# Kernel optimization log

Measured on AMD Instinct MI355X. Metric: run time of the kernel, lower is better.

Reference implementation:

```python
import jax, jax.numpy as jnp
import numpy as np

N = 50000
E = 800000
D_IN = 96
D_OUT = 128


def setup_inputs() -> dict:
    key = jax.random.key(0)
    k1, k2, k3, k4, k5 = jax.random.split(key, 5)
    x = jax.random.normal(k1, (N, D_IN), dtype=jnp.float32)
    edge_index = jax.random.randint(k2, (2, E), 0, N, dtype=jnp.int32)
    s = 1.0 / np.sqrt(D_IN)
    # lin_l: applied to aggregated neighbor features (has bias in PyG SAGEConv)
    W_l = jax.random.uniform(k3, (D_OUT, D_IN), jnp.float32, -s, s)
    b_l = jax.random.uniform(k4, (D_OUT,), jnp.float32, -s, s)
    # lin_r: root/self weight (no bias)
    W_r = jax.random.uniform(k5, (D_OUT, D_IN), jnp.float32, -s, s)
    return {"x": x, "edge_index": edge_index, "W_l": W_l, "b_l": b_l, "W_r": W_r}


def reference(x, edge_index, W_l, b_l, W_r):
    src, dst = edge_index[0], edge_index[1]
    # gather source features, mean-aggregate onto targets
    msg = x[src]  # [E, D_IN]
    summed = jax.ops.segment_sum(msg, dst, num_segments=N)  # [N, D_IN]
    count = jax.ops.segment_sum(jnp.ones((E,), x.dtype), dst, num_segments=N)
    agg = summed / jnp.maximum(count, 1.0)[:, None]
    # SAGEConv: lin_l(agg) + lin_r(x), then layer-level ReLU
    out = agg @ W_l.T + b_l + x @ W_r.T
    return jax.nn.relu(out)
```

## Files before the change

### kernel.cpp

```cpp
#include <hip/hip_runtime.h>
#include <hip/hip_bf16.h>

#define N_NODES 50000
#define N_EDGES 800000
#define D_IN 96
#define D_OUT 128
#define CAP 64

#define N_BINS 256
#define NODES_PER_BIN 196
#define BIN_CAP 4096
#define TAIL_STRIDE 16

#define PART_EPB 3125
#define PART_BLOCKS (N_EDGES / PART_EPB)
#define PART_SLOTS 13

#define CONV_THREADS (N_NODES * 12)
#define CONV_BLOCKS ((CONV_THREADS + 255) / 256)
#define WCONV_BLOCKS 12

#define SLICES 8
#define NODES_PER_SLICE 6250
#define NPB 64
#define SLICE_AG_BLOCKS ((NODES_PER_SLICE + NPB - 1) / NPB)
#define AG_BLOCKS (SLICES * SLICE_AG_BLOCKS)
#define AH_PITCH 104

typedef unsigned short u16;
typedef __attribute__((ext_vector_type(8))) short short8;
typedef __attribute__((ext_vector_type(4))) float f32x4;

__device__ __forceinline__ u16 f2bf(float f) {
    unsigned u = __float_as_uint(f);
    unsigned r = (u + 0x7FFFu + ((u >> 16) & 1u)) >> 16;
    return (u16)r;
}
__device__ __forceinline__ float bf2f(u16 h) {
    return __uint_as_float(((unsigned)h) << 16);
}

__global__ __launch_bounds__(256) void sage_part_conv(
    const int* __restrict__ src,
    const int* __restrict__ dst,
    const float* __restrict__ x,
    const float* __restrict__ Wl,
    const float* __restrict__ Wr,
    int* __restrict__ tail,
    unsigned* __restrict__ binbuf,
    u16* __restrict__ xh,
    u16* __restrict__ Wfrag)
{
    __shared__ unsigned hist[N_BINS];
    __shared__ unsigned base[N_BINS];
    __shared__ unsigned cur[N_BINS];

    const int b = blockIdx.x;
    const int tid = (int)threadIdx.x;

    if (b < PART_BLOCKS) {
        hist[tid] = 0u; cur[tid] = 0u;
        __syncthreads();

        const int ebase = b * PART_EPB;
        const int e0 = ebase + tid;
        int d[PART_SLOTS], s[PART_SLOTS], bn[PART_SLOTS];
#pragma unroll
        for (int i = 0; i < PART_SLOTS; i++) {
            int valid = (tid + i * 256) < PART_EPB;
            int e = valid ? (e0 + i * 256) : ebase;
            d[i] = dst[e];
            s[i] = src[e];
        }
#pragma unroll
        for (int i = 0; i < PART_SLOTS; i++) {
            bn[i] = d[i] / NODES_PER_BIN;
            if ((tid + i * 256) < PART_EPB)
                atomicAdd(&hist[bn[i]], 1u);
        }
        __syncthreads();
        base[tid] = (unsigned)atomicAdd(&tail[tid * TAIL_STRIDE], (int)hist[tid]);
        __syncthreads();
#pragma unroll
        for (int i = 0; i < PART_SLOTS; i++) {
            if ((tid + i * 256) < PART_EPB) {
                unsigned loc = atomicAdd(&cur[bn[i]], 1u);
                unsigned pos = base[bn[i]] + loc;
                unsigned dl = (unsigned)(d[i] - bn[i] * NODES_PER_BIN);
                if (pos < BIN_CAP)
                    binbuf[(unsigned)bn[i] * BIN_CAP + pos] =
                        (dl << 16) | (unsigned)s[i];
            }
        }
    } else if (b < PART_BLOCKS + CONV_BLOCKS) {
        unsigned t = (unsigned)(b - PART_BLOCKS) * 256u + threadIdx.x;
        if (t >= (unsigned)CONV_THREADS) return;
        unsigned n = t / 12u;
        unsigned c8 = t - n * 12u;
        const float* p = x + (size_t)n * D_IN + c8 * 8u;
        short8 v;
#pragma unroll
        for (int i = 0; i < 8; i++) v[i] = (short)f2bf(p[i]);
        *(short8*)(xh + (size_t)n * D_IN + c8 * 8u) = v;
    } else {
        int idx = (b - PART_BLOCKS - CONV_BLOCKS) * 256 + tid;
        int j = idx / 24;
        int c8 = idx - j * 24;
        int kc = c8 >> 2;
        int quad = c8 & 3;
        const float* wsrc = (c8 < 12) ? (Wl + (size_t)j * D_IN + c8 * 8)
                                      : (Wr + (size_t)j * D_IN + (c8 - 12) * 8);
        int jt = j >> 4;
        int col = j & 15;
        short8 v;
#pragma unroll
        for (int i = 0; i < 8; i++) v[i] = (short)f2bf(wsrc[i]);
        *(short8*)(Wfrag + (((jt * 6 + kc) * 64) + col + 16 * quad) * 8) = v;
    }
}

__global__ __launch_bounds__(256) void sage_bin(
    const int* __restrict__ tail,
    const unsigned* __restrict__ binbuf,
    int* __restrict__ cursor,
    u16* __restrict__ bucket)
{
    __shared__ __align__(16) u16 bkt[NODES_PER_BIN * CAP];
    __shared__ unsigned cnt[NODES_PER_BIN];

    const int j = blockIdx.x;
    const int tid = (int)threadIdx.x;
    const int nbase = j * NODES_PER_BIN;
    const int nvalid = (N_NODES - nbase) < NODES_PER_BIN ? (N_NODES - nbase)
                                                         : NODES_PER_BIN;

    for (int r = tid; r < NODES_PER_BIN; r += 256) cnt[r] = 0u;
    __syncthreads();

    int TAIL = tail[j * TAIL_STRIDE];
    if (TAIL > BIN_CAP) TAIL = BIN_CAP;
    const unsigned* sb = binbuf + (size_t)j * BIN_CAP;

    for (int e0 = tid * 4; e0 < TAIL; e0 += 1024) {
        uint4 v = *(const uint4*)(sb + e0);
        unsigned vv0 = v.x, vv1 = v.y, vv2 = v.z, vv3 = v.w;
#pragma unroll
        for (int k = 0; k < 4; k++) {
            unsigned w = (k == 0) ? vv0 : (k == 1) ? vv1 : (k == 2) ? vv2 : vv3;
            if (e0 + k < TAIL) {
                unsigned r = w >> 16;
                if (r < NODES_PER_BIN) {
                    unsigned p = atomicAdd(&cnt[r], 1u);
                    if (p < CAP) bkt[r * CAP + p] = (u16)(w & 0xFFFFu);
                }
            }
        }
    }
    __syncthreads();

    for (int idx = tid; idx < nvalid * 8; idx += 256) {
        int r = idx >> 3, q = idx & 7;
        *(short8*)(bucket + (size_t)(nbase + r) * CAP + q * 8) =
            *(const short8*)(bkt + r * CAP + q * 8);
    }
    for (int r = tid; r < nvalid; r += 256)
        cursor[nbase + r] = (int)cnt[r];
}

__global__ __launch_bounds__(256) void sage_agg_gemm(
    const u16* __restrict__ xh,
    const int* __restrict__ cursor,
    const u16* __restrict__ bucket,
    const u16* __restrict__ Wfrag,
    const float* __restrict__ bl,
    float* __restrict__ out)
{
    __shared__ u16 Ah[NPB * AH_PITCH];

    const int tid = threadIdx.x;
    const int g = blockIdx.x & 7;
    const int kblk = blockIdx.x >> 3;
    const int n0 = g * NODES_PER_SLICE + kblk * NPB;
    const int hi_s = (g + 1) * NODES_PER_SLICE;

#pragma unroll
    for (int rep = 0; rep < 3; rep++) {
        int task = rep * 256 + tid;
        int m = task / 12;
        int c8 = task - m * 12;
        int n = n0 + m;

        float acc[8];
#pragma unroll
        for (int i = 0; i < 8; i++) acc[i] = 0.0f;
        float invd = 0.0f;

        if (n < hi_s) {
            int deg = cursor[n];
            int degc = deg < CAP ? deg : CAP;
            const u16* brow = bucket + (size_t)n * CAP;
            int e = 0;
            for (; e + 8 <= degc; e += 8) {
                short8 id = *(const short8*)(brow + e);
                short8 v[8];
#pragma unroll
                for (int q = 0; q < 8; q++) {
                    unsigned s = (u16)id[q];
                    v[q] = *(const short8*)(xh + s * (unsigned)D_IN + c8 * 8u);
                }
#pragma unroll
                for (int q = 0; q < 8; q++)
#pragma unroll
                    for (int i = 0; i < 8; i++) acc[i] += bf2f((u16)v[q][i]);
            }
            if (e + 4 <= degc) {
                unsigned s0 = brow[e + 0];
                unsigned s1 = brow[e + 1];
                unsigned s2 = brow[e + 2];
                unsigned s3 = brow[e + 3];
                short8 v0 = *(const short8*)(xh + s0 * (unsigned)D_IN + c8 * 8u);
                short8 v1 = *(const short8*)(xh + s1 * (unsigned)D_IN + c8 * 8u);
                short8 v2 = *(const short8*)(xh + s2 * (unsigned)D_IN + c8 * 8u);
                short8 v3 = *(const short8*)(xh + s3 * (unsigned)D_IN + c8 * 8u);
#pragma unroll
                for (int i = 0; i < 8; i++)
                    acc[i] += bf2f((u16)v0[i]) + bf2f((u16)v1[i])
                            + bf2f((u16)v2[i]) + bf2f((u16)v3[i]);
                e += 4;
            }
            for (; e < degc; e++) {
                unsigned s = brow[e];
                short8 v = *(const short8*)(xh + s * (unsigned)D_IN + c8 * 8u);
#pragma unroll
                for (int i = 0; i < 8; i++) acc[i] += bf2f((u16)v[i]);
            }
            invd = 1.0f / fmaxf((float)deg, 1.0f);
        }

        short8 o;
#pragma unroll
        for (int i = 0; i < 8; i++) o[i] = (short)f2bf(acc[i] * invd);
        *(short8*)(Ah + m * AH_PITCH + c8 * 8) = o;
    }
    __syncthreads();

    const int wave = tid >> 6;
    const int lane = tid & 63;
    const int m16 = lane & 15;
    const int quad = lane >> 4;
    const int tilebase = n0 + wave * 16;
    if (tilebase >= hi_s) return;

    int nn = tilebase + m16;
    nn = nn < hi_s ? nn : hi_s - 1;

    const u16* arow = Ah + (wave * 16 + m16) * AH_PITCH + quad * 8;
    const u16* xrow = xh + (size_t)nn * D_IN + quad * 8;
    short8 a[6];
#pragma unroll
    for (int kc = 0; kc < 3; kc++) a[kc]     = *(const short8*)(arow + kc * 32);
#pragma unroll
    for (int kc = 0; kc < 3; kc++) a[3 + kc] = *(const short8*)(xrow + kc * 32);

#pragma unroll
    for (int jt = 0; jt < 8; jt++) {
        f32x4 acc = {0.0f, 0.0f, 0.0f, 0.0f};
#pragma unroll
        for (int kc = 0; kc < 6; kc++) {
            short8 bfrag = *(const short8*)(Wfrag + ((jt * 6 + kc) * 64 + lane) * 8);
            acc = __builtin_amdgcn_mfma_f32_16x16x32_bf16(a[kc], bfrag, acc, 0, 0, 0);
        }
        const int j = jt * 16 + m16;
        const float bj = bl[j];
#pragma unroll
        for (int r = 0; r < 4; r++) {
            int row = quad * 4 + r;
            int n = tilebase + row;
            if (n < hi_s)
                out[(size_t)n * D_OUT + j] = fmaxf(acc[r] + bj, 0.0f);
        }
    }
}

extern "C" void kernel_launch(void* const* d_in, const int* in_sizes, int n_in,
                              void* d_out, int out_size, void* d_ws, size_t ws_size,
                              hipStream_t stream) {
    const float* x   = (const float*)d_in[0];
    const int* eidx  = (const int*)d_in[1];
    const float* Wl  = (const float*)d_in[2];
    const float* bl  = (const float*)d_in[3];
    const float* Wr  = (const float*)d_in[4];
    float* out = (float*)d_out;

    const int* src = eidx;
    const int* dst = eidx + N_EDGES;

    char* ws = (char*)d_ws;
    int*      tailp  = (int*)ws;
    unsigned* binbuf = (unsigned*)(ws + 16384);
    u16*      bucket = (u16*)(ws + 4210688);
    u16*      xh     = (u16*)(ws + 10610688);
    u16*      Wfrag  = (u16*)(ws + 20210688);
    int*      cursor = (int*)(ws + 20259840);

    hipMemsetAsync(tailp, 0, N_BINS * TAIL_STRIDE * sizeof(int), stream);

    {
        dim3 grid(PART_BLOCKS + CONV_BLOCKS + WCONV_BLOCKS);
        sage_part_conv<<<grid, 256, 0, stream>>>(src, dst, x, Wl, Wr,
                                                 tailp, binbuf, xh, Wfrag);
    }
    {
        dim3 grid(N_BINS);
        sage_bin<<<grid, 256, 0, stream>>>(tailp, binbuf, cursor, bucket);
    }
    {
        dim3 grid(AG_BLOCKS);
        sage_agg_gemm<<<grid, 256, 0, stream>>>(xh, cursor, bucket, Wfrag, bl, out);
    }
}
```

Measured before the change: 130.9 us.

## Fuse bucketing into aggregation kernel using per-block partition sub-buckets

The partition kernel now writes edges into fixed-capacity per-(bin, partition-block) slots of 64-node bins, with a per-slot count array. This replaces the global tail atomics and the memset. The separate bin kernel is removed: each aggregation block gathers its 64 nodes' edges from the 256 sub-slots into shared-memory buckets and then aggregates. This drops one kernel launch, the global bucket/cursor round trip and the atomics, at the cost of capping each sub-slot at 24 edges (silent truncation if exceeded) and larger scattered binbuf writes.

```diff
diff --git a/kernel.cpp b/kernel.cpp
--- a/kernel.cpp
+++ b/kernel.cpp
@@ -7,11 +7,9 @@
 #define D_OUT 128
 #define CAP 64
 
-#define N_BINS 256
-#define NODES_PER_BIN 196
-#define BIN_CAP 4096
-#define TAIL_STRIDE 16
-
+#define NPB 64
+#define N_BINS ((N_NODES + NPB - 1) / NPB)
+#define CAP_SUB 24
 #define PART_EPB 3125
 #define PART_BLOCKS (N_EDGES / PART_EPB)
 #define PART_SLOTS 13
@@ -20,11 +18,7 @@
 #define CONV_BLOCKS ((CONV_THREADS + 255) / 256)
 #define WCONV_BLOCKS 12
 
-#define SLICES 8
-#define NODES_PER_SLICE 6250
-#define NPB 64
-#define SLICE_AG_BLOCKS ((NODES_PER_SLICE + NPB - 1) / NPB)
-#define AG_BLOCKS (SLICES * SLICE_AG_BLOCKS)
+#define AG_BLOCKS N_BINS
 #define AH_PITCH 104
 
 typedef unsigned short u16;
@@ -46,25 +40,24 @@
     const float* __restrict__ x,
     const float* __restrict__ Wl,
     const float* __restrict__ Wr,
-    int* __restrict__ tail,
+    u16* __restrict__ cnts,
     unsigned* __restrict__ binbuf,
     u16* __restrict__ xh,
     u16* __restrict__ Wfrag)
 {
     __shared__ unsigned hist[N_BINS];
-    __shared__ unsigned base[N_BINS];
     __shared__ unsigned cur[N_BINS];
 
     const int b = blockIdx.x;
     const int tid = (int)threadIdx.x;
 
     if (b < PART_BLOCKS) {
-        hist[tid] = 0u; cur[tid] = 0u;
+        for (int i = tid; i < N_BINS; i += 256) { hist[i] = 0u; cur[i] = 0u; }
         __syncthreads();
 
         const int ebase = b * PART_EPB;
         const int e0 = ebase + tid;
-        int d[PART_SLOTS], s[PART_SLOTS], bn[PART_SLOTS];
+        int d[PART_SLOTS], s[PART_SLOTS];
 #pragma unroll
         for (int i = 0; i < PART_SLOTS; i++) {
             int valid = (tid + i * 256) < PART_EPB;
@@ -74,22 +67,21 @@
         }
 #pragma unroll
         for (int i = 0; i < PART_SLOTS; i++) {
-            bn[i] = d[i] / NODES_PER_BIN;
             if ((tid + i * 256) < PART_EPB)
-                atomicAdd(&hist[bn[i]], 1u);
+                atomicAdd(&hist[d[i] >> 6], 1u);
         }
         __syncthreads();
-        base[tid] = (unsigned)atomicAdd(&tail[tid * TAIL_STRIDE], (int)hist[tid]);
-        __syncthreads();
+        for (int i = tid; i < N_BINS; i += 256)
+            cnts[(size_t)i * PART_BLOCKS + b] = (u16)hist[i];
 #pragma unroll
         for (int i = 0; i < PART_SLOTS; i++) {
             if ((tid + i * 256) < PART_EPB) {
-                unsigned loc = atomicAdd(&cur[bn[i]], 1u);
-                unsigned pos = base[bn[i]] + loc;
-                unsigned dl = (unsigned)(d[i] - bn[i] * NODES_PER_BIN);
-                if (pos < BIN_CAP)
-                    binbuf[(unsigned)bn[i] * BIN_CAP + pos] =
-                        (dl << 16) | (unsigned)s[i];
+                int bn = d[i] >> 6;
+                unsigned dl = (unsigned)(d[i] & 63);
+                unsigned loc = atomicAdd(&cur[bn], 1u);
+                if (loc < CAP_SUB)
+                    binbuf[((unsigned)bn * PART_BLOCKS + (unsigned)b) * CAP_SUB
+                           + loc] = (dl << 16) | (unsigned)s[i];
             }
         }
     } else if (b < PART_BLOCKS + CONV_BLOCKS) {
@@ -119,69 +111,49 @@
     }
 }
 
-__global__ __launch_bounds__(256) void sage_bin(
-    const int* __restrict__ tail,
-    const unsigned* __restrict__ binbuf,
-    int* __restrict__ cursor,
-    u16* __restrict__ bucket)
-{
-    __shared__ __align__(16) u16 bkt[NODES_PER_BIN * CAP];
-    __shared__ unsigned cnt[NODES_PER_BIN];
-
-    const int j = blockIdx.x;
-    const int tid = (int)threadIdx.x;
-    const int nbase = j * NODES_PER_BIN;
-    const int nvalid = (N_NODES - nbase) < NODES_PER_BIN ? (N_NODES - nbase)
-                                                         : NODES_PER_BIN;
-
-    for (int r = tid; r < NODES_PER_BIN; r += 256) cnt[r] = 0u;
-    __syncthreads();
-
-    int TAIL = tail[j * TAIL_STRIDE];
-    if (TAIL > BIN_CAP) TAIL = BIN_CAP;
-    const unsigned* sb = binbuf + (size_t)j * BIN_CAP;
-
-    for (int e0 = tid * 4; e0 < TAIL; e0 += 1024) {
-        uint4 v = *(const uint4*)(sb + e0);
-        unsigned vv0 = v.x, vv1 = v.y, vv2 = v.z, vv3 = v.w;
-#pragma unroll
-        for (int k = 0; k < 4; k++) {
-            unsigned w = (k == 0) ? vv0 : (k == 1) ? vv1 : (k == 2) ? vv2 : vv3;
-            if (e0 + k < TAIL) {
-                unsigned r = w >> 16;
-                if (r < NODES_PER_BIN) {
-                    unsigned p = atomicAdd(&cnt[r], 1u);
-                    if (p < CAP) bkt[r * CAP + p] = (u16)(w & 0xFFFFu);
-                }
-            }
-        }
-    }
-    __syncthreads();
-
-    for (int idx = tid; idx < nvalid * 8; idx += 256) {
-        int r = idx >> 3, q = idx & 7;
-        *(short8*)(bucket + (size_t)(nbase + r) * CAP + q * 8) =
-            *(const short8*)(bkt + r * CAP + q * 8);
-    }
-    for (int r = tid; r < nvalid; r += 256)
-        cursor[nbase + r] = (int)cnt[r];
-}
-
 __global__ __launch_bounds__(256) void sage_agg_gemm(
     const u16* __restrict__ xh,
-    const int* __restrict__ cursor,
-    const u16* __restrict__ bucket,
+    const u16* __restrict__ cnts,
+    const unsigned* __restrict__ binbuf,
     const u16* __restrict__ Wfrag,
     const float* __restrict__ bl,
     float* __restrict__ out)
 {
+    __shared__ __align__(16) u16 bkt[NPB * CAP];
+    __shared__ unsigned cnt_l[NPB];
     __shared__ u16 Ah[NPB * AH_PITCH];
 
-    const int tid = threadIdx.x;
-    const int g = blockIdx.x & 7;
-    const int kblk = blockIdx.x >> 3;
-    const int n0 = g * NODES_PER_SLICE + kblk * NPB;
-    const int hi_s = (g + 1) * NODES_PER_SLICE;
+    const int j = blockIdx.x;
+    const int tid = (int)threadIdx.x;
+    const int n0 = j * NPB;
+
+    if (tid < NPB) cnt_l[tid] = 0u;
+    __syncthreads();
+
+    {
+        unsigned cnt_t = cnts[(size_t)j * PART_BLOCKS + tid];
+        const uint4* sc = (const uint4*)(binbuf
+                          + ((size_t)j * PART_BLOCKS + tid) * CAP_SUB);
+        uint4 q0 = sc[0], q1 = sc[1], q2 = sc[2], q3 = sc[3], q4 = sc[4], q5 = sc[5];
+        unsigned buf[CAP_SUB];
+        buf[0]=q0.x;  buf[1]=q0.y;  buf[2]=q0.z;  buf[3]=q0.w;
+        buf[4]=q1.x;  buf[5]=q1.y;  buf[6]=q1.z;  buf[7]=q1.w;
+        buf[8]=q2.x;  buf[9]=q2.y;  buf[10]=q2.z; buf[11]=q2.w;
+        buf[12]=q3.x; buf[13]=q3.y; buf[14]=q3.z; buf[15]=q3.w;
+        buf[16]=q4.x; buf[17]=q4.y; buf[18]=q4.z; buf[19]=q4.w;
+        buf[20]=q5.x; buf[21]=q5.y; buf[22]=q5.z; buf[23]=q5.w;
+        unsigned lim = cnt_t < CAP_SUB ? cnt_t : CAP_SUB;
+#pragma unroll
+        for (int e = 0; e < CAP_SUB; e++) {
+            if ((unsigned)e < lim) {
+                unsigned w = buf[e];
+                unsigned r = w >> 16;
+                unsigned p = atomicAdd(&cnt_l[r], 1u);
+                if (p < CAP) bkt[r * CAP + p] = (u16)(w & 0xFFFFu);
+            }
+        }
+    }
+    __syncthreads();
 
 #pragma unroll
     for (int rep = 0; rep < 3; rep++) {
@@ -195,10 +167,10 @@
         for (int i = 0; i < 8; i++) acc[i] = 0.0f;
         float invd = 0.0f;
 
-        if (n < hi_s) {
-            int deg = cursor[n];
+        if (n < N_NODES) {
+            int deg = (int)cnt_l[m];
             int degc = deg < CAP ? deg : CAP;
-            const u16* brow = bucket + (size_t)n * CAP;
+            const u16* brow = bkt + m * CAP;
             int e = 0;
             for (; e + 8 <= degc; e += 8) {
                 short8 id = *(const short8*)(brow + e);
@@ -249,10 +221,10 @@
     const int m16 = lane & 15;
     const int quad = lane >> 4;
     const int tilebase = n0 + wave * 16;
-    if (tilebase >= hi_s) return;
+    if (tilebase >= N_NODES) return;
 
     int nn = tilebase + m16;
-    nn = nn < hi_s ? nn : hi_s - 1;
+    nn = nn < N_NODES ? nn : N_NODES - 1;
 
     const u16* arow = Ah + (wave * 16 + m16) * AH_PITCH + quad * 8;
     const u16* xrow = xh + (size_t)nn * D_IN + quad * 8;
@@ -270,14 +242,14 @@
             short8 bfrag = *(const short8*)(Wfrag + ((jt * 6 + kc) * 64 + lane) * 8);
             acc = __builtin_amdgcn_mfma_f32_16x16x32_bf16(a[kc], bfrag, acc, 0, 0, 0);
         }
-        const int j = jt * 16 + m16;
-        const float bj = bl[j];
+        const int jj = jt * 16 + m16;
+        const float bj = bl[jj];
 #pragma unroll
         for (int r = 0; r < 4; r++) {
             int row = quad * 4 + r;
             int n = tilebase + row;
-            if (n < hi_s)
-                out[(size_t)n * D_OUT + j] = fmaxf(acc[r] + bj, 0.0f);
+            if (n < N_NODES)
+                out[(size_t)n * D_OUT + jj] = fmaxf(acc[r] + bj, 0.0f);
         }
     }
 }
@@ -296,26 +268,18 @@
     const int* dst = eidx + N_EDGES;
 
     char* ws = (char*)d_ws;
-    int*      tailp  = (int*)ws;
-    unsigned* binbuf = (unsigned*)(ws + 16384);
-    u16*      bucket = (u16*)(ws + 4210688);
-    u16*      xh     = (u16*)(ws + 10610688);
-    u16*      Wfrag  = (u16*)(ws + 20210688);
-    int*      cursor = (int*)(ws + 20259840);
-
-    hipMemsetAsync(tailp, 0, N_BINS * TAIL_STRIDE * sizeof(int), stream);
+    unsigned* binbuf = (unsigned*)ws;
+    u16*      cnts   = (u16*)(ws + 19218432);
+    u16*      xh     = (u16*)(ws + 19618816);
+    u16*      Wfrag  = (u16*)(ws + 29218816);
 
     {
         dim3 grid(PART_BLOCKS + CONV_BLOCKS + WCONV_BLOCKS);
         sage_part_conv<<<grid, 256, 0, stream>>>(src, dst, x, Wl, Wr,
-                                                 tailp, binbuf, xh, Wfrag);
-    }
-    {
-        dim3 grid(N_BINS);
-        sage_bin<<<grid, 256, 0, stream>>>(tailp, binbuf, cursor, bucket);
+                                                 cnts, binbuf, xh, Wfrag);
     }
     {
         dim3 grid(AG_BLOCKS);
-        sage_agg_gemm<<<grid, 256, 0, stream>>>(xh, cursor, bucket, Wfrag, bl, out);
-    }
-}
+        sage_agg_gemm<<<grid, 256, 0, stream>>>(xh, cnts, binbuf, Wfrag, bl, out);
+    }
+}
```

Measured after the change: 123.8 us (median of 2 runs). -5.4%, faster.
